# Kernel optimization log

Hardware: AMD Instinct MI355X
Metric: run time of the kernel (lower is better)

Reference implementation:

```python
import jax, jax.numpy as jnp
import numpy as np

B, Q, K, D, H = 4, 2048, 2048, 512, 8
DH = D // H
MASK_VAL = -1e6


def setup_inputs() -> dict:
    key = jax.random.key(0)
    ks = jax.random.split(key, 8)
    queries = jax.random.normal(ks[0], (B, Q, D), dtype=jnp.float32)
    keys = jax.random.normal(ks[1], (B, K, D), dtype=jnp.float32)
    values = jax.random.normal(ks[2], (B, K, D), dtype=jnp.float32)
    valid_lens = jax.random.randint(ks[3], (B,), 1, K + 1, dtype=jnp.int32)
    # torch nn.Linear weights: shape [out_features, in_features], y = x @ W.T
    s = 1.0 / np.sqrt(D)
    W_q = jax.random.uniform(ks[4], (D, D), jnp.float32, -s, s)
    W_k = jax.random.uniform(ks[5], (D, D), jnp.float32, -s, s)
    W_v = jax.random.uniform(ks[6], (D, D), jnp.float32, -s, s)
    W_o = jax.random.uniform(ks[7], (D, D), jnp.float32, -s, s)
    return {"queries": queries, "keys": keys, "values": values,
            "valid_lens": valid_lens, "W_q": W_q, "W_k": W_k,
            "W_v": W_v, "W_o": W_o}


def _split_heads(x):
    # [B, S, D] -> [B, H, S, DH]
    b, s, _ = x.shape
    return x.reshape(b, s, H, DH).transpose(0, 2, 1, 3)


def reference(queries, keys, values, valid_lens, W_q, W_k, W_v, W_o):
    q = _split_heads(queries @ W_q.T)   # [B,H,Q,DH]
    k = _split_heads(keys @ W_k.T)      # [B,H,K,DH]
    v = _split_heads(values @ W_v.T)    # [B,H,K,DH]
    scores = jnp.einsum("bhqd,bhkd->bhqk", q, k) / jnp.sqrt(jnp.float32(DH))
    # padding mask: key position < valid_len[b], broadcast over heads & queries
    mask = jnp.arange(K)[None, None, None, :] < valid_lens[:, None, None, None]
    scores = jnp.where(mask, scores, MASK_VAL)
    attn = jax.nn.softmax(scores, axis=-1)  # dropout=eval/no-op
    out = jnp.einsum("bhqk,bhkd->bhqd", attn, v)
    out = out.transpose(0, 2, 1, 3).reshape(queries.shape[0], q.shape[2], D)
    return out @ W_o.T
```

## Files before the change

kernel.cpp:

```cpp
#include <hip/hip_runtime.h>
#include <cstdint>
#include <cstddef>

#define BB  4
#define QQ  2048
#define SK  2048
#define DD  512
#define HH  8
#define DHH 64
#define CS  16
#define ZMAX 2

typedef __bf16 bf16;
typedef bf16  bf16x8 __attribute__((ext_vector_type(8)));
typedef bf16  bf16x4 __attribute__((ext_vector_type(4)));
typedef float f32x4  __attribute__((ext_vector_type(4)));
typedef _Float16 f16;
typedef f16   f16x4 __attribute__((ext_vector_type(4)));
typedef f16   f16x8 __attribute__((ext_vector_type(8)));

__device__ __forceinline__ void async16(void* lds, const void* g) {
  __builtin_amdgcn_global_load_lds(
      (const __attribute__((address_space(1))) unsigned int*)g,
      (__attribute__((address_space(3))) unsigned int*)lds, 16, 0, 0);
}

__device__ __forceinline__ uint32_t pk2(float lo, float hi) {
  return __builtin_amdgcn_perm(__builtin_bit_cast(uint32_t, hi),
                               __builtin_bit_cast(uint32_t, lo), 0x07060302u);
}

__global__ __launch_bounds__(256) void cvt_all(
    const float* __restrict__ q, const float* __restrict__ k,
    const float* __restrict__ v, const float* __restrict__ w0,
    const float* __restrict__ w1, const float* __restrict__ w2,
    const float* __restrict__ w3, bf16* __restrict__ dq,
    bf16* __restrict__ dk, bf16* __restrict__ dv, bf16* __restrict__ dw0,
    bf16* __restrict__ dw1, bf16* __restrict__ dw2, bf16* __restrict__ dw3,
    int nx4, int nw4) {
  int i = blockIdx.x * 256 + threadIdx.x;
  const float* s;
  bf16* d;
  if (i < nx4)               { s = q;  d = dq;  }
  else if (i < 2 * nx4)      { s = k;  d = dk;  i -= nx4; }
  else if (i < 3 * nx4)      { s = v;  d = dv;  i -= 2 * nx4; }
  else {
    int j = i - 3 * nx4;
    if (j < nw4)             { s = w0; d = dw0; }
    else if (j < 2 * nw4)    { s = w1; d = dw1; j -= nw4; }
    else if (j < 3 * nw4)    { s = w2; d = dw2; j -= 2 * nw4; }
    else if (j < 4 * nw4)    { s = w3; d = dw3; j -= 3 * nw4; }
    else return;
    i = j;
  }
  float4 vv = ((const float4*)s)[i];
  bf16x4 o;
  o[0] = (bf16)vv.x; o[1] = (bf16)vv.y; o[2] = (bf16)vv.z; o[3] = (bf16)vv.w;
  ((bf16x4*)d)[i] = o;
}

template <int MT, typename EpiF>
__device__ __forceinline__ void gemm_body(
    const bf16* __restrict__ A, const bf16* __restrict__ B,
    int tM, int tN, EpiF epi_fn) {
  __shared__ __align__(16) bf16 lA[MT * 32 * 64];
  __shared__ __align__(16) bf16 lB[128 * 64];
  const int tid  = threadIdx.x;
  const int l    = tid & 63;
  const int w    = tid >> 6;
  const int lrow = l & 15, lq = l >> 4;
  const int wm = (w >> 1) * (MT * 16), wn = (w & 1) * 64;

  f32x4 acc[MT][4] = {};
  for (int it = 0; it < 8; ++it) {
    const int kt = it * 64;
    if (it) __syncthreads();
#pragma unroll
    for (int j = 0; j < MT; ++j) {
      int c = j * 256 + tid, row = c >> 3, gcc = (c & 7) ^ (row & 7);
      async16(&lA[c * 8], &A[(size_t)(tM + row) * DD + kt + gcc * 8]);
    }
#pragma unroll
    for (int j = 0; j < 4; ++j) {
      int c = j * 256 + tid, row = c >> 3, gcc = (c & 7) ^ (row & 7);
      async16(&lB[c * 8], &B[(size_t)(tN + row) * DD + kt + gcc * 8]);
    }
    __syncthreads();

#pragma unroll
    for (int ks = 0; ks < 2; ++ks) {
      bf16x8 af[MT], bfr[4];
#pragma unroll
      for (int mt = 0; mt < MT; ++mt) {
        int row = wm + mt * 16 + lrow;
        int chunk = row * 8 + ((ks * 4 + lq) ^ (lrow & 7));
        af[mt] = *(const bf16x8*)&lA[chunk * 8];
      }
#pragma unroll
      for (int nt = 0; nt < 4; ++nt) {
        int row = wn + nt * 16 + lrow;
        int chunk = row * 8 + ((ks * 4 + lq) ^ (lrow & 7));
        bfr[nt] = *(const bf16x8*)&lB[chunk * 8];
      }
#pragma unroll
      for (int mt = 0; mt < MT; ++mt)
#pragma unroll
        for (int nt = 0; nt < 4; ++nt)
          acc[mt][nt] = __builtin_amdgcn_mfma_f32_16x16x32_bf16(
              af[mt], bfr[nt], acc[mt][nt], 0, 0, 0);
    }
  }

#pragma unroll
  for (int mt = 0; mt < MT; ++mt)
#pragma unroll
    for (int nt = 0; nt < 4; ++nt) {
      int row0 = tM + wm + mt * 16 + lq * 4;
      int col  = tN + wn + nt * 16 + lrow;
      epi_fn(acc[mt][nt], row0, col);
    }
}

__global__ __launch_bounds__(256, 3) void proj3(
    const bf16* __restrict__ xq, const bf16* __restrict__ wq, bf16* __restrict__ qh,
    const bf16* __restrict__ xk, const bf16* __restrict__ wk, bf16* __restrict__ kh,
    const bf16* __restrict__ xv, const bf16* __restrict__ wv, bf16* __restrict__ vt,
    float qscale) {
  const int z = blockIdx.y, x = blockIdx.x;
  if (z < 2) {
    const bf16* A  = z == 0 ? wq : wk;
    const bf16* B  = z == 0 ? xq : xk;
    bf16* Cout     = z == 0 ? qh : kh;
    const float scale = z == 0 ? qscale : 1.0f;
    int tM = (x & 3) * 128, tN = (x >> 2) * 128;
    gemm_body<4>(A, B, tM, tN, [&](const f32x4& a, int row0, int col) {
      int b2 = col >> 11, s = col & 2047;
      int h2 = row0 >> 6, dh0 = row0 & 63;
      bf16x4 o;
#pragma unroll
      for (int r = 0; r < 4; ++r) o[r] = (bf16)(a[r] * scale);
      *(bf16x4*)&Cout[((size_t)(b2 * HH + h2) * QQ + s) * DHH + dh0] = o;
    });
  } else {
    int tM = (x >> 2) * 128, tN = (x & 3) * 128;
    gemm_body<4>(xv, wv, tM, tN, [&](const f32x4& a, int row0, int col) {
      int b2 = row0 >> 11, s0 = row0 & 2047;
      int h2 = col >> 6,  dh = col & 63;
      int tile = s0 >> 6, kk = s0 & 63;
      int g = kk >> 4, a2 = (kk >> 2) & 3;
      int idx0 = ((g >> 1) * 4 + a2) * 8 + (g & 1) * 4;
      bf16x4 o;
#pragma unroll
      for (int r = 0; r < 4; ++r) o[r] = (bf16)a[r];
      *(bf16x4*)&vt[((size_t)(b2 * HH + h2) * DHH + dh) * SK + tile * 64 + idx0] = o;
    });
  }
}

__global__ __launch_bounds__(256, 3) void proj_o(
    const bf16* __restrict__ wo, const bf16* __restrict__ ao,
    float* __restrict__ Cout) {
  const int x = blockIdx.x;
  int tM = (x & 7) * 64, tN = (x >> 3) * 128;
  gemm_body<2>(wo, ao, tM, tN, [&](const f32x4& a, int row0, int col) {
    *(float4*)&Cout[(size_t)col * DD + row0] = *(const float4*)&a;
  });
}

__global__ __launch_bounds__(256, 4) void attn_split(
    const bf16* __restrict__ qh, const bf16* __restrict__ kh,
    const bf16* __restrict__ vt, const int* __restrict__ valid_lens,
    f16* __restrict__ opart, float* __restrict__ lpart) {
  __shared__ __align__(16) bf16 lK[2][64 * 64];
  __shared__ __align__(16) bf16 lV[2][64 * 64];
  const int tid  = threadIdx.x;
  const int l    = tid & 63;
  const int w    = tid >> 6;
  const int lrow = l & 15, lq = l >> 4;
  const int rx   = lrow & 7;
  const int bh = blockIdx.x;
  const int b = bh >> 3;
  const int qt = blockIdx.y, z = blockIdx.z;
  const int vl  = valid_lens[b];
  const int nkt = (vl + 63) >> 6;
  const int kt0 = z * CS;
  const int kt1 = min(nkt, kt0 + CS);
  const size_t pbase = ((size_t)bh * 16 + qt) * ZMAX + z;
  float* lout = lpart + pbase * 128;
  f16*   oout = opart + pbase * 8192;

  if (kt0 >= kt1) {
    if (tid < 128) lout[tid] = 0.f;
    return;
  }

  const int q0 = qt * 128 + w * 32;
  const bf16* qbase = qh + (size_t)bh * QQ * DHH;
  const bf16* kbase = kh + (size_t)bh * SK * DHH;
  const bf16* vbase = vt + (size_t)bh * DHH * SK;

  bf16x8 qf[2][2];
#pragma unroll
  for (int g = 0; g < 2; ++g)
#pragma unroll
    for (int ks = 0; ks < 2; ++ks)
      qf[g][ks] = *(const bf16x8*)
          &qbase[(size_t)(q0 + g * 16 + lrow) * DHH + ks * 32 + lq * 8];

  auto stageKV = [&](int k0, int buf) {
#pragma unroll
    for (int j = 0; j < 2; ++j) {
      int c = j * 256 + tid, row = c >> 3, gcc = (c & 7) ^ (row & 7);
      async16(&lK[buf][c * 8], &kbase[(size_t)(k0 + row) * DHH + gcc * 8]);
    }
#pragma unroll
    for (int j = 0; j < 2; ++j) {
      int c = j * 256 + tid, row = c >> 3, gcc = (c & 7) ^ (row & 7);
      async16(&lV[buf][c * 8], &vbase[(size_t)row * SK + k0 + gcc * 8]);
    }
  };

  f32x4 acc[2][4] = {};
  float rs[2] = {0.f, 0.f};

  stageKV(kt0 * 64, kt0 & 1);
  for (int kt = kt0; kt < kt1; ++kt) {
    __syncthreads();
    if (kt + 1 < kt1) stageKV((kt + 1) * 64, (kt + 1) & 1);
    const bf16* bufK = lK[kt & 1];
    const bf16* bufV = lV[kt & 1];
    const int k0 = kt * 64;

    f32x4 s[2][4] = {};
#pragma unroll
    for (int ks = 0; ks < 2; ++ks) {
#pragma unroll
      for (int t = 0; t < 4; ++t) {
        int row = t * 16 + lrow;
        int chunkc = row * 8 + ((ks * 4 + lq) ^ rx);
        bf16x8 kf = *(const bf16x8*)&bufK[chunkc * 8];
#pragma unroll
        for (int g = 0; g < 2; ++g)
          s[g][t] = __builtin_amdgcn_mfma_f32_16x16x32_bf16(
              kf, qf[g][ks], s[g][t], 0, 0, 0);
      }
    }

    if (vl < k0 + 64) {
#pragma unroll
      for (int t = 0; t < 4; ++t) {
        int kb = k0 + t * 16 + lq * 4;
#pragma unroll
        for (int r = 0; r < 4; ++r)
          if (kb + r >= vl) { s[0][t][r] = -1e30f; s[1][t][r] = -1e30f; }
      }
    }

#pragma unroll
    for (int g = 0; g < 2; ++g)
#pragma unroll
      for (int t = 0; t < 4; ++t)
#pragma unroll
        for (int r = 0; r < 4; ++r) {
          float p = __builtin_amdgcn_exp2f(s[g][t][r]);
          rs[g] += p;
          s[g][t][r] = p;
        }

#pragma unroll
    for (int p2 = 0; p2 < 2; ++p2) {
      union { bf16x8 v; uint32_t u[4]; } pb[2];
#pragma unroll
      for (int g = 0; g < 2; ++g) {
        pb[g].u[0] = pk2(s[g][2 * p2][0], s[g][2 * p2][1]);
        pb[g].u[1] = pk2(s[g][2 * p2][2], s[g][2 * p2][3]);
        pb[g].u[2] = pk2(s[g][2 * p2 + 1][0], s[g][2 * p2 + 1][1]);
        pb[g].u[3] = pk2(s[g][2 * p2 + 1][2], s[g][2 * p2 + 1][3]);
      }
      int cc = (p2 * 4 + lq) ^ rx;
#pragma unroll
      for (int mt = 0; mt < 4; ++mt) {
        int row = mt * 16 + lrow;
        bf16x8 vf = *(const bf16x8*)&bufV[(row * 8 + cc) * 8];
#pragma unroll
        for (int g = 0; g < 2; ++g)
          acc[g][mt] = __builtin_amdgcn_mfma_f32_16x16x32_bf16(
              vf, pb[g].v, acc[g][mt], 0, 0, 0);
      }
    }
  }

#pragma unroll
  for (int g = 0; g < 2; ++g) {
    rs[g] += __shfl_xor(rs[g], 16);
    rs[g] += __shfl_xor(rs[g], 32);
    if (lq == 0) lout[w * 32 + g * 16 + lrow] = rs[g];
  }

#pragma unroll
  for (int g = 0; g < 2; ++g)
#pragma unroll
    for (int mt = 0; mt < 4; ++mt) {
      f16x4 o;
#pragma unroll
      for (int r = 0; r < 4; ++r) o[r] = (f16)acc[g][mt][r];
      *(f16x4*)&oout[(w * 32 + g * 16 + lrow) * 64 + mt * 16 + lq * 4] = o;
    }
}

__global__ __launch_bounds__(256) void attn_combine(
    const f16* __restrict__ opart, const float* __restrict__ lpart,
    bf16* __restrict__ ao) {
  const int bh = blockIdx.x, qt = blockIdx.y;
  const int b = bh >> 3, h = bh & 7;
  const size_t base = ((size_t)bh * 16 + qt) * ZMAX;
  const int t = threadIdx.x, q = t >> 1, ds = (t & 1) * 32;
  float O[32] = {};
  float lsum = 0.f;
#pragma unroll
  for (int z = 0; z < ZMAX; ++z) {
    float lz = lpart[(base + z) * 128 + q];
    if (lz != 0.f) {
      lsum += lz;
      const f16x8* p = (const f16x8*)&opart[(base + z) * 8192 + q * 64 + ds];
#pragma unroll
      for (int j = 0; j < 4; ++j) {
        f16x8 a = p[j];
#pragma unroll
        for (int r = 0; r < 8; ++r) O[j * 8 + r] += (float)a[r];
      }
    }
  }
  float inv = 1.0f / lsum;
  bf16* dst = &ao[((size_t)(b * QQ + qt * 128 + q)) * DD + h * DHH + ds];
#pragma unroll
  for (int j = 0; j < 4; ++j) {
    bf16x8 o;
#pragma unroll
    for (int r = 0; r < 8; ++r) o[r] = (bf16)(O[j * 8 + r] * inv);
    *(bf16x8*)(dst + j * 8) = o;
  }
}

extern "C" void kernel_launch(void* const* d_in, const int* in_sizes, int n_in,
                              void* d_out, int out_size, void* d_ws, size_t ws_size,
                              hipStream_t stream) {
  const float* queries    = (const float*)d_in[0];
  const float* keys       = (const float*)d_in[1];
  const float* values     = (const float*)d_in[2];
  const int*   valid_lens = (const int*)d_in[3];
  const float* W_q = (const float*)d_in[4];
  const float* W_k = (const float*)d_in[5];
  const float* W_v = (const float*)d_in[6];
  const float* W_o = (const float*)d_in[7];

  const size_t NX = (size_t)BB * QQ * DD;
  const size_t NW = (size_t)DD * DD;

  bf16* xq = (bf16*)d_ws;
  bf16* xk = xq + NX;
  bf16* xv = xk + NX;
  bf16* wq = xv + NX;
  bf16* wk = wq + NW;
  bf16* wv = wk + NW;
  bf16* wo = wv + NW;
  bf16* qh = wo + NW;
  bf16* kh = qh + NX;
  bf16* vt = kh + NX;
  f16*  opart = (f16*)(vt + NX);
  float* lpart = (float*)(opart + (size_t)32 * 16 * ZMAX * 8192);
  bf16* ao = xq;

  dim3 blk(256);
  const int nx4 = (int)(NX / 4), nw4 = (int)(NW / 4);
  const int ncvt = (3 * nx4 + 4 * nw4 + 255) / 256;
  cvt_all<<<dim3(ncvt), blk, 0, stream>>>(
      queries, keys, values, W_q, W_k, W_v, W_o,
      xq, xk, xv, wq, wk, wv, wo, nx4, nw4);

  const float qscale = 0.125f * 1.44269504088896340736f;
  proj3<<<dim3(256, 3), blk, 0, stream>>>(xq, wq, qh, xk, wk, kh, xv, wv, vt,
                                          qscale);

  attn_split<<<dim3(BB * HH, QQ / 128, ZMAX), blk, 0, stream>>>(
      qh, kh, vt, valid_lens, opart, lpart);
  attn_combine<<<dim3(BB * HH, QQ / 128), blk, 0, stream>>>(opart, lpart, ao);

  proj_o<<<dim3(512), blk, 0, stream>>>(wo, ao, (float*)d_out);
}
```

Measured before the change: 183.3 us.

## Load K/V fragments directly from global memory instead of LDS staging

The attention kernel drops the double-buffered LDS staging of K and V tiles, along with its barriers. Each wave now loads its MFMA operand fragments straight from global memory into registers, with V loads issued at the start of each tile. This removes the LDS traffic and the __syncthreads, but the four waves of a block now fetch the same K/V data redundantly, relying on cache hits. Register pressure also rises, and occupancy is lowered from 4 to 3 blocks per CU.

Result: slower. 258.2 us (+40.9%).

```diff
diff --git a/kernel.cpp b/kernel.cpp
--- a/kernel.cpp
+++ b/kernel.cpp
@@ -15,6 +15,7 @@
 typedef bf16  bf16x8 __attribute__((ext_vector_type(8)));
 typedef bf16  bf16x4 __attribute__((ext_vector_type(4)));
 typedef float f32x4  __attribute__((ext_vector_type(4)));
+typedef uint32_t u32x4 __attribute__((ext_vector_type(4)));
 typedef _Float16 f16;
 typedef f16   f16x4 __attribute__((ext_vector_type(4)));
 typedef f16   f16x8 __attribute__((ext_vector_type(8)));
@@ -167,17 +168,14 @@
   });
 }
 
-__global__ __launch_bounds__(256, 4) void attn_split(
+__global__ __launch_bounds__(256, 3) void attn_split(
     const bf16* __restrict__ qh, const bf16* __restrict__ kh,
     const bf16* __restrict__ vt, const int* __restrict__ valid_lens,
     f16* __restrict__ opart, float* __restrict__ lpart) {
-  __shared__ __align__(16) bf16 lK[2][64 * 64];
-  __shared__ __align__(16) bf16 lV[2][64 * 64];
   const int tid  = threadIdx.x;
   const int l    = tid & 63;
   const int w    = tid >> 6;
   const int lrow = l & 15, lq = l >> 4;
-  const int rx   = lrow & 7;
   const int bh = blockIdx.x;
   const int b = bh >> 3;
   const int qt = blockIdx.y, z = blockIdx.z;
@@ -207,38 +205,27 @@
       qf[g][ks] = *(const bf16x8*)
           &qbase[(size_t)(q0 + g * 16 + lrow) * DHH + ks * 32 + lq * 8];
 
-  auto stageKV = [&](int k0, int buf) {
-#pragma unroll
-    for (int j = 0; j < 2; ++j) {
-      int c = j * 256 + tid, row = c >> 3, gcc = (c & 7) ^ (row & 7);
-      async16(&lK[buf][c * 8], &kbase[(size_t)(k0 + row) * DHH + gcc * 8]);
-    }
-#pragma unroll
-    for (int j = 0; j < 2; ++j) {
-      int c = j * 256 + tid, row = c >> 3, gcc = (c & 7) ^ (row & 7);
-      async16(&lV[buf][c * 8], &vbase[(size_t)row * SK + k0 + gcc * 8]);
-    }
-  };
-
   f32x4 acc[2][4] = {};
   float rs[2] = {0.f, 0.f};
 
-  stageKV(kt0 * 64, kt0 & 1);
   for (int kt = kt0; kt < kt1; ++kt) {
-    __syncthreads();
-    if (kt + 1 < kt1) stageKV((kt + 1) * 64, (kt + 1) & 1);
-    const bf16* bufK = lK[kt & 1];
-    const bf16* bufV = lV[kt & 1];
     const int k0 = kt * 64;
 
+    bf16x8 vf[2][4];
+#pragma unroll
+    for (int p2 = 0; p2 < 2; ++p2)
+#pragma unroll
+      for (int mt = 0; mt < 4; ++mt)
+        vf[p2][mt] = *(const bf16x8*)
+            &vbase[(size_t)(mt * 16 + lrow) * SK + k0 + (p2 * 4 + lq) * 8];
+
     f32x4 s[2][4] = {};
 #pragma unroll
     for (int ks = 0; ks < 2; ++ks) {
 #pragma unroll
       for (int t = 0; t < 4; ++t) {
-        int row = t * 16 + lrow;
-        int chunkc = row * 8 + ((ks * 4 + lq) ^ rx);
-        bf16x8 kf = *(const bf16x8*)&bufK[chunkc * 8];
+        bf16x8 kf = *(const bf16x8*)
+            &kbase[(size_t)(k0 + t * 16 + lrow) * DHH + (ks * 4 + lq) * 8];
 #pragma unroll
         for (int g = 0; g < 2; ++g)
           s[g][t] = __builtin_amdgcn_mfma_f32_16x16x32_bf16(
@@ -269,23 +256,22 @@
 
 #pragma unroll
     for (int p2 = 0; p2 < 2; ++p2) {
-      union { bf16x8 v; uint32_t u[4]; } pb[2];
+      u32x4 pu[2];
 #pragma unroll
       for (int g = 0; g < 2; ++g) {
-        pb[g].u[0] = pk2(s[g][2 * p2][0], s[g][2 * p2][1]);
-        pb[g].u[1] = pk2(s[g][2 * p2][2], s[g][2 * p2][3]);
-        pb[g].u[2] = pk2(s[g][2 * p2 + 1][0], s[g][2 * p2 + 1][1]);
-        pb[g].u[3] = pk2(s[g][2 * p2 + 1][2], s[g][2 * p2 + 1][3]);
-      }
-      int cc = (p2 * 4 + lq) ^ rx;
+        pu[g][0] = pk2(s[g][2 * p2][0], s[g][2 * p2][1]);
+        pu[g][1] = pk2(s[g][2 * p2][2], s[g][2 * p2][3]);
+        pu[g][2] = pk2(s[g][2 * p2 + 1][0], s[g][2 * p2 + 1][1]);
+        pu[g][3] = pk2(s[g][2 * p2 + 1][2], s[g][2 * p2 + 1][3]);
+      }
+      bf16x8 pb0 = __builtin_bit_cast(bf16x8, pu[0]);
+      bf16x8 pb1 = __builtin_bit_cast(bf16x8, pu[1]);
 #pragma unroll
       for (int mt = 0; mt < 4; ++mt) {
-        int row = mt * 16 + lrow;
-        bf16x8 vf = *(const bf16x8*)&bufV[(row * 8 + cc) * 8];
-#pragma unroll
-        for (int g = 0; g < 2; ++g)
-          acc[g][mt] = __builtin_amdgcn_mfma_f32_16x16x32_bf16(
-              vf, pb[g].v, acc[g][mt], 0, 0, 0);
+        acc[0][mt] = __builtin_amdgcn_mfma_f32_16x16x32_bf16(
+            vf[p2][mt], pb0, acc[0][mt], 0, 0, 0);
+        acc[1][mt] = __builtin_amdgcn_mfma_f32_16x16x32_bf16(
+            vf[p2][mt], pb1, acc[1][mt], 0, 0, 0);
       }
     }
   }
```
